# Performance work log

Hardware: AMD Instinct MI355X
Metric: run time of the kernel (lower is better)

The kernel has to match this reference:

```python
import math
import jax, jax.numpy as jnp
import numpy as np

B, H, W = 2, 128, 128
HW = H * W
D, NH, NL, KS = 256, 8, 1, 5
NP = KS * KS
HD = D // NH
DFF = 1024
KEEP = 0.25
H_SIZE = 188.0
EPS = 1e-5


def _layernorm(x, g, b):
    m = x.mean(-1, keepdims=True)
    v = ((x - m) ** 2).mean(-1, keepdims=True)
    return (x - m) * jax.lax.rsqrt(v + EPS) * g + b


def _mha(q_in, k_in, v_in, w_qkv, b_qkv, w_o, b_o):
    wq, wk, wv = jnp.split(w_qkv, 3, axis=0)
    bq, bk, bv = jnp.split(b_qkv, 3, axis=0)
    def heads(x, w, b):
        y = x @ w.T + b
        return y.reshape(y.shape[0], y.shape[1], NH, HD)
    q, k, v = heads(q_in, wq, bq), heads(k_in, wk, bk), heads(v_in, wv, bv)
    scores = jnp.einsum('bqhd,bkhd->bhqk', q, k) / math.sqrt(HD)
    attn = jax.nn.softmax(scores, axis=-1)
    out = jnp.einsum('bhqk,bkhd->bqhd', attn, v).reshape(q_in.shape[0], q_in.shape[1], D)
    return out @ w_o.T + b_o


def _bilinear(v, grid):
    # v: (B, HW, NH, HD); grid: (B, LQ, NH, NP, 2) normalized (x, y) in [0,1]
    x = grid[..., 0] * W - 0.5
    y = grid[..., 1] * H - 0.5
    x0 = jnp.floor(x); y0 = jnp.floor(y)
    lx = x - x0; ly = y - y0
    x0i = x0.astype(jnp.int32); y0i = y0.astype(jnp.int32)
    bidx = jnp.arange(v.shape[0])[:, None, None, None]
    hidx = jnp.arange(NH)[None, None, :, None]
    def corner(xi, yi, wgt):
        valid = (xi >= 0) & (xi < W) & (yi >= 0) & (yi < H)  # zero-pad outside
        idx = jnp.clip(yi, 0, H - 1) * W + jnp.clip(xi, 0, W - 1)
        s = v[bidx, idx, hidx]  # (B, LQ, NH, NP, HD)
        return s * (wgt * valid)[..., None]
    return (corner(x0i, y0i, (1 - lx) * (1 - ly))
            + corner(x0i + 1, y0i, lx * (1 - ly))
            + corner(x0i, y0i + 1, (1 - lx) * ly)
            + corner(x0i + 1, y0i + 1, lx * ly))


def _where_to_attend(query, ref_windows, lbw, lbb, sow, sob, kernel_indices):
    Bq, L = ref_windows.shape[:2]
    ob = (query @ lbw.T + lbb).reshape(Bq, L, NH, NL, 4)  # with_rotation=False -> 4 vars
    rw = ref_windows[:, :, None, None, :]  # (B, L, 1, 1, 7)
    ref_boxes = rw[..., jnp.array([0, 1, 3, 4])]
    ref_angles = rw[..., 6:7]
    angles = jnp.broadcast_to(ref_angles, (Bq, L, NH, NL, 1))
    boxes = ref_boxes + ob / 8.0 * ref_boxes[..., jnp.array([2, 3, 2, 3])]
    center = boxes[..., None, :2]  # (B, L, NH, NL, 1, 2)
    size = boxes[..., None, 2:]
    cos_a, sin_a = jnp.cos(angles), jnp.sin(angles)
    rot = jnp.stack([cos_a, -sin_a, sin_a, cos_a], -1).reshape(Bq, L, NH, NL, 1, 2, 2)
    dgrid = (query @ sow.T + sob).reshape(Bq, L, NH, NL, NP, 2) / H_SIZE
    fg = kernel_indices * jax.nn.relu(size)              # (B, L, NH, NL, NP, 2)
    fg = center + (fg[..., None, :] * rot).sum(-1)       # rotate then shift
    return fg + dgrid


def _box_attn(query, value, ref_windows, vpw, vpb, law, lab, lbw, lbb, sow, sob, ow, ob_, kernel_indices):
    Bq, LQ = query.shape[:2]
    LV = value.shape[1]
    v = (value @ vpw.T + vpb).reshape(Bq, LV, NH, HD)
    aw = jax.nn.softmax((query @ law.T + lab).reshape(Bq, LQ, NH, NL * NP), axis=-1)
    aw = aw.reshape(Bq, LQ, NH, NL, NP)
    grid = _where_to_attend(query, ref_windows, lbw, lbb, sow, sob, kernel_indices)
    sampled = _bilinear(v, grid[:, :, :, 0])             # single level (NL=1)
    out = (aw[:, :, :, 0, :, None] * sampled).sum(-2).reshape(Bq, LQ, D)
    return out @ ow.T + ob_


def _forward(src, pos, ref_windows, score_mask, in_proj_w, in_proj_b, mha_out_w, mha_out_b,
             value_proj_w, value_proj_b, linear_attn_w, linear_attn_b, linear_box_w, linear_box_b,
             samp_off_w, samp_off_b, ca_out_w, ca_out_b, lin1_w, lin1_b, lin2_w, lin2_b,
             qn_g, qn_b, n1_g, n1_b, n2_g, n2_b, kernel_indices):
    Bq = src.shape[0]
    fg_num = math.ceil(src.shape[1] * KEEP)
    sel_score, indices = jax.lax.top_k(score_mask, fg_num)
    gather = lambda x, i: jnp.take_along_axis(x, i[..., None], axis=1)
    sel_src = gather(src, indices)
    sel_pos = gather(pos, indices)
    sel_ref = gather(ref_windows, indices)
    q_num = math.ceil(fg_num * KEEP)
    q_idx = jax.lax.top_k(sel_score, q_num)[1]
    q_src = gather(sel_src, q_idx)
    q_pos = gather(sel_pos, q_idx)
    qk = q_src + q_pos
    q2 = _mha(qk, qk, q_src, in_proj_w, in_proj_b, mha_out_w, mha_out_b)
    q_src = _layernorm(q_src + q2, qn_g, qn_b)
    brow = jnp.arange(Bq)[:, None]
    sel_src = sel_src.at[brow, q_idx].set(q_src)
    src2 = _box_attn(sel_src + sel_pos, src, sel_ref, value_proj_w, value_proj_b,
                     linear_attn_w, linear_attn_b, linear_box_w, linear_box_b,
                     samp_off_w, samp_off_b, ca_out_w, ca_out_b, kernel_indices)
    sel_src = _layernorm(sel_src + src2, n1_g, n1_b)
    ff = jax.nn.relu(sel_src @ lin1_w.T + lin1_b) @ lin2_w.T + lin2_b
    sel_src = _layernorm(sel_src + ff, n2_g, n2_b)
    return src.at[brow, indices].set(sel_src)


def setup_inputs() -> dict:
    key = jax.random.key(0)
    ks = jax.random.split(key, 16)
    def w(k, shape):
        return jax.random.normal(k, shape, dtype=jnp.float32) * 0.02
    # deformable sampling-offsets bias init (per-head directional grid)
    thetas = np.arange(NH) * (2.0 * np.pi / NH)
    g = np.stack([np.cos(thetas), np.sin(thetas)], -1)
    g = g / np.abs(g).max(-1, keepdims=True)
    g = np.tile(g.reshape(NH, 1, 1, 2), (1, NL, NP, 1)) * (np.arange(NP) + 1).reshape(1, 1, NP, 1)
    samp_off_b = jnp.asarray(g.reshape(-1), dtype=jnp.float32)
    # fixed kernel indices buffer (odd kernel, (x,y) order, /kernel_size)
    ind = np.linspace(-(KS - 1) / 2, (KS - 1) / 2, KS)
    ii, jj = np.meshgrid(ind, ind, indexing='ij')
    kernel_indices = jnp.asarray(np.stack([jj, ii], -1).reshape(-1, 2) / KS, dtype=jnp.float32)
    return dict(
        src=jax.random.normal(ks[0], (B, HW, D), dtype=jnp.float32),
        pos=jax.random.normal(ks[1], (B, HW, D), dtype=jnp.float32),
        src_shape=jnp.array([[H, W]], dtype=jnp.int32),
        src_start_idx=jnp.zeros((1,), dtype=jnp.int32),
        ref_windows=jax.random.uniform(ks[2], (B, HW, 7), dtype=jnp.float32),
        score_mask=jax.random.normal(ks[3], (B, HW), dtype=jnp.float32),
        in_proj_w=w(ks[4], (3 * D, D)), in_proj_b=jnp.zeros((3 * D,), jnp.float32),
        mha_out_w=w(ks[5], (D, D)), mha_out_b=jnp.zeros((D,), jnp.float32),
        value_proj_w=w(ks[6], (D, D)), value_proj_b=jnp.zeros((D,), jnp.float32),
        linear_attn_w=w(ks[7], (NH * NL * NP, D)), linear_attn_b=jnp.zeros((NH * NL * NP,), jnp.float32),
        linear_box_w=w(ks[8], (NL * NH * 4, D)), linear_box_b=jnp.zeros((NL * NH * 4,), jnp.float32),
        samp_off_w=w(ks[9], (NH * NL * NP * 2, D)), samp_off_b=samp_off_b,
        ca_out_w=w(ks[10], (D, D)), ca_out_b=jnp.zeros((D,), jnp.float32),
        lin1_w=w(ks[11], (DFF, D)), lin1_b=jnp.zeros((DFF,), jnp.float32),
        lin2_w=w(ks[12], (D, DFF)), lin2_b=jnp.zeros((D,), jnp.float32),
        qn_g=jnp.ones((D,), jnp.float32), qn_b=jnp.zeros((D,), jnp.float32),
        n1_g=jnp.ones((D,), jnp.float32), n1_b=jnp.zeros((D,), jnp.float32),
        n2_g=jnp.ones((D,), jnp.float32), n2_b=jnp.zeros((D,), jnp.float32),
        kernel_indices=kernel_indices,
    )


def reference(src, pos, src_shape, src_start_idx, ref_windows, score_mask,
              in_proj_w, in_proj_b, mha_out_w, mha_out_b, value_proj_w, value_proj_b,
              linear_attn_w, linear_attn_b, linear_box_w, linear_box_b, samp_off_w, samp_off_b,
              ca_out_w, ca_out_b, lin1_w, lin1_b, lin2_w, lin2_b,
              qn_g, qn_b, n1_g, n1_b, n2_g, n2_b, kernel_indices):
    # src_shape/src_start_idx are static single-level metadata (H, W closed over)
    return _forward(src, pos, ref_windows, score_mask, in_proj_w, in_proj_b, mha_out_w, mha_out_b,
                    value_proj_w, value_proj_b, linear_attn_w, linear_attn_b, linear_box_w, linear_box_b,
                    samp_off_w, samp_off_b, ca_out_w, ca_out_b, lin1_w, lin1_b, lin2_w, lin2_b,
                    qn_g, qn_b, n1_g, n1_b, n2_g, n2_b, kernel_indices)
```

## Files before the change

kernel.cpp:

```cpp
#include <hip/hip_runtime.h>
#include <hip/hip_bf16.h>
#include <math.h>

#define HW_N   16384
#define DIM    256
#define NSEL   4096
#define NQ     1024
#define NHEAD  8
#define HD     32
#define NP_    25
#define DFF_   1024

#define OFF_SELREF  8448LL
#define OFF_SELSRC  65792LL
#define OFF_SELPOS  2162944LL
#define OFF_QUERY   4260096LL
#define OFF_BIG     6357248LL
#define OFF_WBF     10551552LL
#define OFF_F       14745856LL

__device__ __forceinline__ unsigned int f2s(float f) {
    unsigned int u = __float_as_uint(f);
    return (u & 0x80000000u) ? ~u : (u | 0x80000000u);
}

typedef __bf16 bf16x8 __attribute__((ext_vector_type(8)));
typedef __bf16 bf16x4 __attribute__((ext_vector_type(4)));
typedef float  f32x4  __attribute__((ext_vector_type(4)));

extern "C" __global__ __launch_bounds__(256)
void wcvt_kernel(const float* __restrict__ s0, const float* __restrict__ s1,
                 const float* __restrict__ s2, const float* __restrict__ s3,
                 const float* __restrict__ s4, const float* __restrict__ s5,
                 const float* __restrict__ s6, const float* __restrict__ s7,
                 const float* __restrict__ s8, __hip_bfloat16* __restrict__ dst) {
    const long long g = (long long)blockIdx.x * 256 + threadIdx.x;
    const float* s; long long base;
    if      (g < 196608)  { s = s0; base = 0; }
    else if (g < 262144)  { s = s1; base = 196608; }
    else if (g < 327680)  { s = s2; base = 262144; }
    else if (g < 378880)  { s = s3; base = 327680; }
    else if (g < 387072)  { s = s4; base = 378880; }
    else if (g < 489472)  { s = s5; base = 387072; }
    else if (g < 555008)  { s = s6; base = 489472; }
    else if (g < 817152)  { s = s7; base = 555008; }
    else                  { s = s8; base = 817152; }
    dst[g] = __float2bfloat16(s[g - base]);
}

extern "C" __global__ __launch_bounds__(512)
void topk_hist_kernel(const float* __restrict__ score, unsigned int* __restrict__ hist) {
    const int t = threadIdx.x, bx = blockIdx.x, bb = blockIdx.y;
    const int i = bx * 512 + t;
    unsigned int u = f2s(score[(long long)bb * HW_N + i]);
    atomicAdd(&hist[bb * 8192 + (u >> 19)], 1u);
}

extern "C" __global__ __launch_bounds__(1024)
void topk_scan_kernel(const unsigned int* __restrict__ hist, unsigned int* __restrict__ ctrl) {
    __shared__ unsigned int scan[1024];
    const int t = threadIdx.x, bb = blockIdx.x;
    unsigned int loc[8]; unsigned int lsum = 0u;
    #pragma unroll
    for (int k = 0; k < 8; ++k) { loc[k] = hist[bb * 8192 + t * 8 + k]; lsum += loc[k]; }
    scan[t] = lsum;
    __syncthreads();
    for (int off = 1; off < 1024; off <<= 1) {
        unsigned int v = (t + off < 1024) ? scan[t + off] : 0u;
        __syncthreads();
        scan[t] += v;
        __syncthreads();
    }
    unsigned int nxt = (t < 1023) ? scan[t + 1] : 0u;
    unsigned int run = nxt;
    for (int k = 7; k >= 0; --k) {
        run += loc[k];
        unsigned int above = run - loc[k];
        if (run >= 1024u && above < 1024u) { ctrl[bb * 16 + 0] = (unsigned)(t * 8 + k); ctrl[bb * 16 + 1] = 1024u - above; }
        if (run >= 4096u && above < 4096u) { ctrl[bb * 16 + 2] = (unsigned)(t * 8 + k); ctrl[bb * 16 + 3] = 4096u - above; }
    }
}

extern "C" __global__ __launch_bounds__(1024)
void topk_collect_kernel(const float* __restrict__ score, unsigned int* __restrict__ ctrl,
                         unsigned long long* __restrict__ list1,
                         unsigned long long* __restrict__ list2) {
    const int t = threadIdx.x, bx = blockIdx.x, bb = blockIdx.y;
    const int i = bx * 1024 + t;
    const unsigned int T1 = ctrl[bb * 16 + 0], T2 = ctrl[bb * 16 + 2];
    unsigned int u = f2s(score[(long long)bb * HW_N + i]);
    unsigned int bin = u >> 19;
    unsigned long long key = ((unsigned long long)u << 32) | (unsigned int)(~(unsigned int)i);
    if (bin == T1) {
        unsigned int p = atomicAdd(&ctrl[bb * 16 + 4], 1u);
        if (p < 2048u) list1[bb * 2048 + p] = key;
    }
    if (bin == T2 && T2 != T1) {
        unsigned int p = atomicAdd(&ctrl[bb * 16 + 5], 1u);
        if (p < 2048u) list2[bb * 2048 + p] = key;
    }
}

extern "C" __global__ __launch_bounds__(1024)
void topk_classify_kernel(const float* __restrict__ score, unsigned int* __restrict__ ctrl,
                          const unsigned long long* __restrict__ list1,
                          const unsigned long long* __restrict__ list2,
                          int* __restrict__ idx_out) {
    __shared__ unsigned int cA, cB, baseA, baseB;
    const int t = threadIdx.x, bx = blockIdx.x, bb = blockIdx.y;
    const int i = bx * 1024 + t;
    if (t == 0) { cA = 0u; cB = 0u; }
    __syncthreads();
    const unsigned int T1 = ctrl[bb * 16 + 0], need1 = ctrl[bb * 16 + 1];
    const unsigned int T2 = ctrl[bb * 16 + 2], need2 = ctrl[bb * 16 + 3];
    const unsigned int c1 = min(ctrl[bb * 16 + 4], 2048u);
    const unsigned int c2 = min(ctrl[bb * 16 + 5], 2048u);
    unsigned int u = f2s(score[(long long)bb * HW_N + i]);
    unsigned int bin = u >> 19;
    unsigned long long key = ((unsigned long long)u << 32) | (unsigned int)(~(unsigned int)i);
    bool inA = false, inB = false;
    if (bin > T1) {
        inA = true;
    } else if (bin == T1) {
        unsigned int r = 0;
        for (unsigned int q = 0; q < c1; ++q) r += (list1[bb * 2048 + q] > key) ? 1u : 0u;
        if (r < need1) inA = true;
        else if (T2 == T1) inB = (r < need2);
        else inB = true;
    } else if (bin > T2) {
        inB = true;
    } else if (bin == T2) {
        unsigned int r = 0;
        for (unsigned int q = 0; q < c2; ++q) r += (list2[bb * 2048 + q] > key) ? 1u : 0u;
        inB = (r < need2);
    }
    unsigned int sA = 0u, sB = 0u;
    if (inA) sA = atomicAdd(&cA, 1u);
    if (inB) sB = atomicAdd(&cB, 1u);
    __syncthreads();
    if (t == 0) {
        baseA = atomicAdd(&ctrl[bb * 16 + 6], cA);
        baseB = atomicAdd(&ctrl[bb * 16 + 7], cB);
    }
    __syncthreads();
    if (inA) idx_out[bb * NSEL + baseA + sA] = i;
    if (inB) idx_out[bb * NSEL + 1024 + baseB + sB] = i;
}

extern "C" __global__ __launch_bounds__(256)
void gather_kernel(const float* __restrict__ src, const float* __restrict__ pos,
                   const float* __restrict__ refw, const int* __restrict__ idx,
                   float* __restrict__ selsrc, float* __restrict__ selpos,
                   float* __restrict__ selref, float* __restrict__ qk) {
    const int s = blockIdx.x, bb = blockIdx.y, t = threadIdx.x;
    const int i = idx[bb * NSEL + s];
    const long long so = ((long long)(bb * NSEL + s)) * DIM;
    const long long go = ((long long)(bb * HW_N + i)) * DIM;
    float sv = src[go + t], pv = pos[go + t];
    selsrc[so + t] = sv;
    selpos[so + t] = pv;
    if (s < NQ) qk[((long long)(bb * NQ + s)) * DIM + t] = sv + pv;
    if (t < 7)
        selref[(long long)(bb * NSEL + s) * 7 + t] = refw[(long long)(bb * HW_N + i) * 7 + t];
}

extern "C" __global__ __launch_bounds__(256)
void gemm_kernel(const void* __restrict__ Avp, long long sA,
                 const __hip_bfloat16* __restrict__ W, const float* __restrict__ bias,
                 float* __restrict__ C, long long sC,
                 int M, int N, int K, int relu, int omode, int amode) {
    __shared__ __hip_bfloat16 As[64][72];
    __shared__ __hip_bfloat16 Ws[64][72];
    const int t = threadIdx.x;
    const int n0 = blockIdx.x * 64, m0 = blockIdx.y * 64;
    const long long zoff = (long long)blockIdx.z * sC;
    const int lane = t & 63, wv = t >> 6;
    const int mw = (wv >> 1) * 32, nw = (wv & 1) * 32;
    const int fr = lane & 15;
    const int fk = (lane >> 4) * 8;
    const int sr = t >> 2;
    const int sk = (t & 3) * 16;

    f32x4 acc[2][2];
    #pragma unroll
    for (int i = 0; i < 2; ++i)
        #pragma unroll
        for (int j = 0; j < 2; ++j) acc[i][j] = {0.f, 0.f, 0.f, 0.f};

    const bool wok = (n0 + sr) < N;
    for (int k0 = 0; k0 < K; k0 += 64) {
        uint4 wa = make_uint4(0u, 0u, 0u, 0u), wb = make_uint4(0u, 0u, 0u, 0u);
        if (wok) {
            const __hip_bfloat16* wp = W + (long long)(n0 + sr) * K + k0 + sk;
            wa = *(const uint4*)wp;
            wb = *(const uint4*)(wp + 8);
        }
        if (amode) {
            const __hip_bfloat16* ap = (const __hip_bfloat16*)Avp
                + (long long)blockIdx.z * sA + (long long)(m0 + sr) * K + k0 + sk;
            uint4 aa = *(const uint4*)ap;
            uint4 ab = *(const uint4*)(ap + 8);
            __syncthreads();
            *(uint4*)&As[sr][sk] = aa;
            *(uint4*)&As[sr][sk + 8] = ab;
            *(uint4*)&Ws[sr][sk] = wa;
            *(uint4*)&Ws[sr][sk + 8] = wb;
        } else {
            const float* ap = (const float*)Avp
                + (long long)blockIdx.z * sA + (long long)(m0 + sr) * K + k0 + sk;
            float av[16];
            #pragma unroll
            for (int q = 0; q < 4; ++q) {
                float4 v = *(const float4*)(ap + q * 4);
                av[q * 4 + 0] = v.x; av[q * 4 + 1] = v.y; av[q * 4 + 2] = v.z; av[q * 4 + 3] = v.w;
            }
            __syncthreads();
            #pragma unroll
            for (int q = 0; q < 16; ++q) As[sr][sk + q] = __float2bfloat16(av[q]);
            *(uint4*)&Ws[sr][sk] = wa;
            *(uint4*)&Ws[sr][sk + 8] = wb;
        }
        __syncthreads();
        #pragma unroll
        for (int kk = 0; kk < 64; kk += 32) {
            bf16x8 a0 = *(const bf16x8*)&As[mw + fr][kk + fk];
            bf16x8 a1 = *(const bf16x8*)&As[mw + 16 + fr][kk + fk];
            bf16x8 b0 = *(const bf16x8*)&Ws[nw + fr][kk + fk];
            bf16x8 b1 = *(const bf16x8*)&Ws[nw + 16 + fr][kk + fk];
            acc[0][0] = __builtin_amdgcn_mfma_f32_16x16x32_bf16(a0, b0, acc[0][0], 0, 0, 0);
            acc[0][1] = __builtin_amdgcn_mfma_f32_16x16x32_bf16(a0, b1, acc[0][1], 0, 0, 0);
            acc[1][0] = __builtin_amdgcn_mfma_f32_16x16x32_bf16(a1, b0, acc[1][0], 0, 0, 0);
            acc[1][1] = __builtin_amdgcn_mfma_f32_16x16x32_bf16(a1, b1, acc[1][1], 0, 0, 0);
        }
    }
    const int crow = (lane >> 4) * 4;
    #pragma unroll
    for (int mi = 0; mi < 2; ++mi) {
        #pragma unroll
        for (int ni = 0; ni < 2; ++ni) {
            const int col = n0 + nw + ni * 16 + fr;
            if (col < N) {
                const float bv = bias ? bias[col] : 0.f;
                #pragma unroll
                for (int r = 0; r < 4; ++r) {
                    const int row = m0 + mw + mi * 16 + crow + r;
                    float v = acc[mi][ni][r] + bv;
                    if (relu) v = fmaxf(v, 0.f);
                    if (omode == 0) {
                        C[zoff + (long long)row * N + col] = v;
                    } else if (omode == 1) {
                        ((__hip_bfloat16*)C)[zoff + (long long)row * N + col] = __float2bfloat16(v);
                    } else if (omode == 2) {
                        ((__hip_bfloat16*)C)[zoff + (long long)col * M + row] = __float2bfloat16(v);
                    } else {
                        ((__hip_bfloat16*)C)[zoff + ((long long)(col >> 5) * 16384 + row) * 32 + (col & 31)]
                            = __float2bfloat16(v);
                    }
                }
            }
        }
    }
}

extern "C" __global__ __launch_bounds__(256)
void attn_kernel(const __hip_bfloat16* __restrict__ qkb,
                 const __hip_bfloat16* __restrict__ vT,
                 float* __restrict__ attout) {
    __shared__ __hip_bfloat16 pb[16][1048];
    __shared__ float redm[4][16];
    __shared__ float reds[4][16];
    __shared__ float redo[4][16][33];
    const int t = threadIdx.x;
    const int qt = blockIdx.x, h = blockIdx.y, bb = blockIdx.z;
    const int q0 = qt * 16;
    const int lane = t & 63, wv = t >> 6;
    const int fr = lane & 15, g = lane >> 4;
    const int kbase = wv * 256;
    const float scale = 0.17677669529663687f;

    bf16x8 qfrag = *(const bf16x8*)(qkb + ((long long)(bb * NQ + q0 + fr)) * 512 + h * HD + g * 8);

    f32x4 sfr[16];
    #pragma unroll
    for (int kt = 0; kt < 16; ++kt) {
        const int key0 = kbase + kt * 16;
        bf16x8 kf = *(const bf16x8*)(qkb + ((long long)(bb * NQ + key0 + fr)) * 512 + 256 + h * HD + g * 8);
        f32x4 z = {0.f, 0.f, 0.f, 0.f};
        sfr[kt] = __builtin_amdgcn_mfma_f32_16x16x32_bf16(qfrag, kf, z, 0, 0, 0);
    }
    #pragma unroll
    for (int kt = 0; kt < 16; ++kt)
        #pragma unroll
        for (int r = 0; r < 4; ++r) sfr[kt][r] *= scale;

    #pragma unroll
    for (int r = 0; r < 4; ++r) {
        float mx = -1e30f;
        #pragma unroll
        for (int kt = 0; kt < 16; ++kt) mx = fmaxf(mx, sfr[kt][r]);
        #pragma unroll
        for (int mm = 1; mm <= 8; mm <<= 1) mx = fmaxf(mx, __shfl_xor(mx, mm, 64));
        float sm = 0.f;
        #pragma unroll
        for (int kt = 0; kt < 16; ++kt) sm += expf(sfr[kt][r] - mx);
        #pragma unroll
        for (int mm = 1; mm <= 8; mm <<= 1) sm += __shfl_xor(sm, mm, 64);
        if (fr == 0) { redm[wv][4 * g + r] = mx; reds[wv][4 * g + r] = sm; }
    }
    __syncthreads();

    float gm[4], gl[4];
    #pragma unroll
    for (int r = 0; r < 4; ++r) {
        const int q = 4 * g + r;
        float mm = fmaxf(fmaxf(redm[0][q], redm[1][q]), fmaxf(redm[2][q], redm[3][q]));
        float ll = 0.f;
        #pragma unroll
        for (int w2 = 0; w2 < 4; ++w2) ll += reds[w2][q] * expf(redm[w2][q] - mm);
        gm[r] = mm; gl[r] = 1.f / ll;
    }
    #pragma unroll
    for (int kt = 0; kt < 16; ++kt) {
        #pragma unroll
        for (int r = 0; r < 4; ++r) {
            float p = expf(sfr[kt][r] - gm[r]) * gl[r];
            pb[4 * g + r][kbase + kt * 16 + fr] = __float2bfloat16(p);
        }
    }

    f32x4 o0 = {0.f, 0.f, 0.f, 0.f}, o1 = {0.f, 0.f, 0.f, 0.f};
    const __hip_bfloat16* vbase = vT + ((long long)bb * DIM + h * HD) * 1024;
    #pragma unroll
    for (int ks = 0; ks < 8; ++ks) {
        const int key0 = kbase + ks * 32 + g * 8;
        bf16x8 pf = *(const bf16x8*)&pb[fr][key0];
        bf16x8 v0 = *(const bf16x8*)(vbase + (long long)fr * 1024 + key0);
        bf16x8 v1 = *(const bf16x8*)(vbase + (long long)(16 + fr) * 1024 + key0);
        o0 = __builtin_amdgcn_mfma_f32_16x16x32_bf16(pf, v0, o0, 0, 0, 0);
        o1 = __builtin_amdgcn_mfma_f32_16x16x32_bf16(pf, v1, o1, 0, 0, 0);
    }

    #pragma unroll
    for (int r = 0; r < 4; ++r) {
        redo[wv][4 * g + r][fr] = o0[r];
        redo[wv][4 * g + r][16 + fr] = o1[r];
    }
    __syncthreads();
    #pragma unroll
    for (int i = 0; i < 2; ++i) {
        const int idx = t + i * 256;
        const int q = idx >> 5, d = idx & 31;
        float v = redo[0][q][d] + redo[1][q][d] + redo[2][q][d] + redo[3][q][d];
        attout[((long long)(bb * NQ + q0 + q)) * DIM + h * HD + d] = v;
    }
}

extern "C" __global__ __launch_bounds__(256)
void ln_kernel(const float* __restrict__ X, long long sx,
               const float* __restrict__ R, long long sr,
               const float* __restrict__ g, const float* __restrict__ bta,
               float* __restrict__ O, long long so) {
    __shared__ float red[4];
    const int row = blockIdx.x, bb = blockIdx.y, t = threadIdx.x;
    float x = X[(long long)bb * sx + (long long)row * DIM + t]
            + R[(long long)bb * sr + (long long)row * DIM + t];
    float v = x;
    #pragma unroll
    for (int m = 32; m >= 1; m >>= 1) v += __shfl_xor(v, m, 64);
    if ((t & 63) == 0) red[t >> 6] = v;
    __syncthreads();
    float mean = (red[0] + red[1] + red[2] + red[3]) * (1.f / 256.f);
    __syncthreads();
    float d = x - mean;
    v = d * d;
    #pragma unroll
    for (int m = 32; m >= 1; m >>= 1) v += __shfl_xor(v, m, 64);
    if ((t & 63) == 0) red[t >> 6] = v;
    __syncthreads();
    float var = (red[0] + red[1] + red[2] + red[3]) * (1.f / 256.f);
    O[(long long)bb * so + (long long)row * DIM + t] = d * rsqrtf(var + 1e-5f) * g[t] + bta[t];
}

extern "C" __global__ __launch_bounds__(256)
void addq_kernel(const float* __restrict__ a, const float* __restrict__ b2, float* __restrict__ o) {
    long long i = (long long)blockIdx.x * 256 + threadIdx.x;
    o[i] = a[i] + b2[i];
}

extern "C" __global__ __launch_bounds__(256)
void boxattn_kernel(const float* __restrict__ aw, const float* __restrict__ ob,
                    const float* __restrict__ dgrid, const float* __restrict__ selref,
                    const __hip_bfloat16* __restrict__ vp, const float* __restrict__ kidx,
                    float* __restrict__ boxout) {
    __shared__ float aw_s[200];
    __shared__ float ob_s[32];
    __shared__ float ref_s[7];
    __shared__ float ki_s[50];
    __shared__ float box_s[8][6];
    __shared__ float mx_s[8];
    __shared__ float inv_s[8];
    __shared__ float wq_s[200];
    __shared__ int   i4_s[800];
    __shared__ float w4_s[800];
    __shared__ float red4[4][8][32];
    const int t = threadIdx.x;
    const int s = blockIdx.x, bb = blockIdx.y;
    const long long base = (long long)(bb * NSEL + s);
    if (t < 200) aw_s[t] = aw[base * 200 + t];
    if (t < 32)  ob_s[t] = ob[base * 32 + t];
    if (t < 7)   ref_s[t] = selref[base * 7 + t];
    if (t < 50)  ki_s[t] = kidx[t];
    __syncthreads();

    if (t < 8) {
        float mx = -1e30f;
        #pragma unroll
        for (int p = 0; p < NP_; ++p) mx = fmaxf(mx, aw_s[t * NP_ + p]);
        mx_s[t] = mx;
        const float r0 = ref_s[0], r1 = ref_s[1], r3 = ref_s[3], r4 = ref_s[4], r6 = ref_s[6];
        box_s[t][0] = r0 + ob_s[t * 4 + 0] * 0.125f * r3;
        box_s[t][1] = r1 + ob_s[t * 4 + 1] * 0.125f * r4;
        box_s[t][2] = fmaxf(r3 + ob_s[t * 4 + 2] * 0.125f * r3, 0.f);
        box_s[t][3] = fmaxf(r4 + ob_s[t * 4 + 3] * 0.125f * r4, 0.f);
        box_s[t][4] = cosf(r6);
        box_s[t][5] = sinf(r6);
    }
    __syncthreads();

    if (t < 200) {
        const int h = t / NP_, p = t - h * NP_;
        const float w = expf(aw_s[t] - mx_s[h]);
        wq_s[t] = w;
        const float cx = box_s[h][0], cy = box_s[h][1];
        const float sw = box_s[h][2], sh = box_s[h][3];
        const float ca = box_s[h][4], sa = box_s[h][5];
        const float fx = ki_s[p * 2 + 0] * sw;
        const float fy = ki_s[p * 2 + 1] * sh;
        const float gx = cx + ca * fx - sa * fy + dgrid[base * 400 + 2 * t + 0] * (1.f / 188.f);
        const float gy = cy + sa * fx + ca * fy + dgrid[base * 400 + 2 * t + 1] * (1.f / 188.f);
        const float x = gx * 128.f - 0.5f;
        const float y = gy * 128.f - 0.5f;
        const float x0f = floorf(x), y0f = floorf(y);
        const float lx = x - x0f, ly = y - y0f;
        const int x0 = (int)x0f, y0 = (int)y0f;
        #pragma unroll
        for (int c = 0; c < 4; ++c) {
            const int xi = x0 + (c & 1);
            const int yi = y0 + (c >> 1);
            const float wgt = ((c & 1) ? lx : 1.f - lx) * ((c >> 1) ? ly : 1.f - ly);
            const bool valid = (xi >= 0) & (xi < 128) & (yi >= 0) & (yi < 128);
            const int cxi = min(max(xi, 0), 127);
            const int cyi = min(max(yi, 0), 127);
            i4_s[t * 4 + c] = cyi * 128 + cxi;
            w4_s[t * 4 + c] = w * (valid ? wgt : 0.f);
        }
    }
    __syncthreads();
    if (t < 8) {
        float sm = 0.f;
        #pragma unroll
        for (int p = 0; p < NP_; ++p) sm += wq_s[t * NP_ + p];
        inv_s[t] = 1.f / sm;
    }
    __syncthreads();

    {
        const int lane = t & 63, wv = t >> 6;
        const int h2 = lane >> 3, q = lane & 7;
        const __hip_bfloat16* vb = vp + ((long long)(bb * 8 + h2) * 16384) * 32 + q * 4;
        int   pix[25];
        float wls[25];
        #pragma unroll
        for (int u = 0; u < 25; ++u) {
            const int e = h2 * 100 + wv + u * 4;
            pix[u] = i4_s[e];
            wls[u] = w4_s[e];
        }
        bf16x4 vv[25];
        #pragma unroll
        for (int u = 0; u < 25; ++u)
            vv[u] = *(const bf16x4*)(vb + (long long)pix[u] * 32);
        __builtin_amdgcn_sched_barrier(0);
        float a0 = 0.f, a1 = 0.f, a2 = 0.f, a3 = 0.f;
        #pragma unroll
        for (int u = 0; u < 25; ++u) {
            a0 += wls[u] * (float)vv[u][0];
            a1 += wls[u] * (float)vv[u][1];
            a2 += wls[u] * (float)vv[u][2];
            a3 += wls[u] * (float)vv[u][3];
        }
        red4[wv][h2][q * 4 + 0] = a0;
        red4[wv][h2][q * 4 + 1] = a1;
        red4[wv][h2][q * 4 + 2] = a2;
        red4[wv][h2][q * 4 + 3] = a3;
    }
    __syncthreads();
    {
        const int h = t >> 5, d = t & 31;
        float v = red4[0][h][d] + red4[1][h][d] + red4[2][h][d] + red4[3][h][d];
        boxout[base * DIM + h * HD + d] = v * inv_s[h];
    }
}

extern "C" __global__ __launch_bounds__(256)
void scatter_kernel(const int* __restrict__ idx, const float* __restrict__ sel,
                    float* __restrict__ out) {
    const int s = blockIdx.x, bb = blockIdx.y, t = threadIdx.x;
    const int i = idx[bb * NSEL + s];
    out[((long long)(bb * HW_N + i)) * DIM + t] = sel[((long long)(bb * NSEL + s)) * DIM + t];
}

extern "C" void kernel_launch(void* const* d_in, const int* in_sizes, int n_in,
                              void* d_out, int out_size, void* d_ws, size_t ws_size,
                              hipStream_t stream) {
    const float* src          = (const float*)d_in[0];
    const float* pos          = (const float*)d_in[1];
    const float* refw         = (const float*)d_in[4];
    const float* score        = (const float*)d_in[5];
    const float* in_proj_w    = (const float*)d_in[6];
    const float* in_proj_b    = (const float*)d_in[7];
    const float* mha_out_w    = (const float*)d_in[8];
    const float* mha_out_b    = (const float*)d_in[9];
    const float* value_proj_w = (const float*)d_in[10];
    const float* value_proj_b = (const float*)d_in[11];
    const float* lin_attn_w   = (const float*)d_in[12];
    const float* lin_attn_b   = (const float*)d_in[13];
    const float* lin_box_w    = (const float*)d_in[14];
    const float* lin_box_b    = (const float*)d_in[15];
    const float* samp_off_w   = (const float*)d_in[16];
    const float* samp_off_b   = (const float*)d_in[17];
    const float* ca_out_w     = (const float*)d_in[18];
    const float* ca_out_b     = (const float*)d_in[19];
    const float* lin1_w       = (const float*)d_in[20];
    const float* lin1_b       = (const float*)d_in[21];
    const float* lin2_w       = (const float*)d_in[22];
    const float* lin2_b       = (const float*)d_in[23];
    const float* qn_g         = (const float*)d_in[24];
    const float* qn_b         = (const float*)d_in[25];
    const float* n1_g         = (const float*)d_in[26];
    const float* n1_b         = (const float*)d_in[27];
    const float* n2_g         = (const float*)d_in[28];
    const float* n2_b         = (const float*)d_in[29];
    const float* kidx         = (const float*)d_in[30];

    float* w = (float*)d_ws;
    int* idxp = (int*)d_ws;
    float* selref = w + OFF_SELREF;
    float* selsrc = w + OFF_SELSRC;
    float* selpos = w + OFF_SELPOS;
    float* boxout = w + OFF_SELPOS;
    float* query  = w + OFF_QUERY;
    float* src2   = w + OFF_QUERY;
    __hip_bfloat16* vproj  = (__hip_bfloat16*)(w + OFF_BIG);
    __hip_bfloat16* ffntb  = (__hip_bfloat16*)(w + OFF_BIG);
    __hip_bfloat16* wbf    = (__hip_bfloat16*)(w + OFF_WBF);
    float* qk     = w + OFF_F;
    __hip_bfloat16* qkb = (__hip_bfloat16*)(w + OFF_F + 524288);
    __hip_bfloat16* vT  = (__hip_bfloat16*)(w + OFF_F + 1572864);
    float* attout = w + OFF_F + 2097152;
    float* q2     = w + OFF_F + 2621440;
    float* aw     = w + OFF_F;
    float* obuf   = w + OFF_F + 1638400;
    float* dgrid  = w + OFF_F + 1900544;
    float* ff     = w + OFF_F;
    unsigned int* hist2 = (unsigned int*)(w + OFF_F);
    unsigned int* ctrl2 = hist2 + 16384;
    unsigned long long* list1 = (unsigned long long*)(hist2 + 16448);
    unsigned long long* list2 = list1 + 2 * 2048;
    float* out    = (float*)d_out;

    const long long W_INPROJ = 0, W_MHAOUT = 196608, W_VALUE = 262144,
                    W_LATTN = 327680, W_LBOX = 378880, W_SOFF = 387072,
                    W_CAOUT = 489472, W_LIN1 = 555008, W_LIN2 = 817152;

    hipMemcpyAsync(d_out, src, (size_t)2 * HW_N * DIM * sizeof(float),
                   hipMemcpyDeviceToDevice, stream);

    wcvt_kernel<<<4216, 256, 0, stream>>>(in_proj_w, mha_out_w, value_proj_w,
                                          lin_attn_w, lin_box_w, samp_off_w,
                                          ca_out_w, lin1_w, lin2_w, wbf);

    hipMemsetAsync(hist2, 0, 16448 * sizeof(unsigned int), stream);
    topk_hist_kernel<<<dim3(32, 2), 512, 0, stream>>>(score, hist2);
    topk_scan_kernel<<<2, 1024, 0, stream>>>(hist2, ctrl2);
    topk_collect_kernel<<<dim3(16, 2), 1024, 0, stream>>>(score, ctrl2, list1, list2);
    topk_classify_kernel<<<dim3(16, 2), 1024, 0, stream>>>(score, ctrl2, list1, list2, idxp);

    gather_kernel<<<dim3(NSEL, 2), 256, 0, stream>>>(src, pos, refw, idxp,
                                                     selsrc, selpos, selref, qk);
    gemm_kernel<<<dim3(8, 16, 2), 256, 0, stream>>>(qk, 262144LL, wbf + W_INPROJ, in_proj_b,
                                                    (float*)qkb, 524288LL, NQ, 512, 256, 0, 1, 0);
    gemm_kernel<<<dim3(4, 16, 2), 256, 0, stream>>>(selsrc, 1048576LL, wbf + W_INPROJ + 512 * 256,
                                                    in_proj_b + 512, (float*)vT, 262144LL, NQ, 256, 256, 0, 2, 0);
    attn_kernel<<<dim3(64, 8, 2), 256, 0, stream>>>(qkb, vT, attout);
    gemm_kernel<<<dim3(4, 16, 2), 256, 0, stream>>>(attout, 262144LL, wbf + W_MHAOUT, mha_out_b,
                                                    q2, 262144LL, NQ, 256, 256, 0, 0, 0);
    ln_kernel<<<dim3(NQ, 2), 256, 0, stream>>>(selsrc, 1048576LL, q2, 262144LL,
                                               qn_g, qn_b, selsrc, 1048576LL);
    addq_kernel<<<8192, 256, 0, stream>>>(selsrc, selpos, query);
    gemm_kernel<<<dim3(4, 256, 2), 256, 0, stream>>>(src, 4194304LL, wbf + W_VALUE, value_proj_b,
                                                     (float*)vproj, 4194304LL, HW_N, 256, 256, 0, 3, 0);
    gemm_kernel<<<dim3(4, 64, 2), 256, 0, stream>>>(query, 1048576LL, wbf + W_LATTN, lin_attn_b,
                                                    aw, 819200LL, NSEL, 200, 256, 0, 0, 0);
    gemm_kernel<<<dim3(1, 64, 2), 256, 0, stream>>>(query, 1048576LL, wbf + W_LBOX, lin_box_b,
                                                    obuf, 131072LL, NSEL, 32, 256, 0, 0, 0);
    gemm_kernel<<<dim3(7, 64, 2), 256, 0, stream>>>(query, 1048576LL, wbf + W_SOFF, samp_off_b,
                                                    dgrid, 1638400LL, NSEL, 400, 256, 0, 0, 0);
    boxattn_kernel<<<dim3(NSEL, 2), 256, 0, stream>>>(aw, obuf, dgrid, selref, vproj, kidx, boxout);
    gemm_kernel<<<dim3(4, 64, 2), 256, 0, stream>>>(boxout, 1048576LL, wbf + W_CAOUT, ca_out_b,
                                                    src2, 1048576LL, NSEL, 256, 256, 0, 0, 0);
    ln_kernel<<<dim3(NSEL, 2), 256, 0, stream>>>(selsrc, 1048576LL, src2, 1048576LL,
                                                 n1_g, n1_b, selsrc, 1048576LL);
    gemm_kernel<<<dim3(16, 64, 2), 256, 0, stream>>>(selsrc, 1048576LL, wbf + W_LIN1, lin1_b,
                                                     (float*)ffntb, 4194304LL, NSEL, DFF_, 256, 1, 1, 0);
    gemm_kernel<<<dim3(4, 64, 2), 256, 0, stream>>>(ffntb, 4194304LL, wbf + W_LIN2, lin2_b,
                                                    ff, 1048576LL, NSEL, 256, DFF_, 0, 0, 1);
    ln_kernel<<<dim3(NSEL, 2), 256, 0, stream>>>(selsrc, 1048576LL, ff, 1048576LL,
                                                 n2_g, n2_b, selsrc, 1048576LL);
    scatter_kernel<<<dim3(NSEL, 2), 256, 0, stream>>>(idxp, selsrc, out);
}
```

Before: 457.1 us.

## Alias attention LDS buffers, batch loads before MFMA, reuse softmax exponentials

The attention kernel now shares one LDS buffer between the probability tile and the output-reduction scratch, with an added barrier to separate the two uses. This lowers shared memory per block, and launch bounds now request 4 blocks per CU. K and V/P fragment loads are grouped ahead of their MFMAs behind sched_barrier so memory latency can overlap. Softmax keeps the exponentials from the first pass and rescales them, using fast __expf, instead of recomputing exp. This adds register pressure from the batched fragments and slightly changes numerics.

```diff
diff --git a/kernel.cpp b/kernel.cpp
--- a/kernel.cpp
+++ b/kernel.cpp
@@ -262,14 +262,15 @@
     }
 }
 
-extern "C" __global__ __launch_bounds__(256)
+extern "C" __global__ __launch_bounds__(256, 4)
 void attn_kernel(const __hip_bfloat16* __restrict__ qkb,
                  const __hip_bfloat16* __restrict__ vT,
                  float* __restrict__ attout) {
-    __shared__ __hip_bfloat16 pb[16][1048];
+    __shared__ float sbuf[8256];
     __shared__ float redm[4][16];
     __shared__ float reds[4][16];
-    __shared__ float redo[4][16][33];
+    __hip_bfloat16 (*pb)[1032] = (__hip_bfloat16 (*)[1032])sbuf;
+    float (*redo)[16][33] = (float (*)[16][33])sbuf;
     const int t = threadIdx.x;
     const int qt = blockIdx.x, h = blockIdx.y, bb = blockIdx.z;
     const int q0 = qt * 16;
@@ -282,17 +283,26 @@
 
     f32x4 sfr[16];
     #pragma unroll
-    for (int kt = 0; kt < 16; ++kt) {
-        const int key0 = kbase + kt * 16;
-        bf16x8 kf = *(const bf16x8*)(qkb + ((long long)(bb * NQ + key0 + fr)) * 512 + 256 + h * HD + g * 8);
-        f32x4 z = {0.f, 0.f, 0.f, 0.f};
-        sfr[kt] = __builtin_amdgcn_mfma_f32_16x16x32_bf16(qfrag, kf, z, 0, 0, 0);
+    for (int half = 0; half < 2; ++half) {
+        bf16x8 kf[8];
+        #pragma unroll
+        for (int j = 0; j < 8; ++j) {
+            const int key0 = kbase + (half * 8 + j) * 16;
+            kf[j] = *(const bf16x8*)(qkb + ((long long)(bb * NQ + key0 + fr)) * 512 + 256 + h * HD + g * 8);
+        }
+        __builtin_amdgcn_sched_barrier(0);
+        #pragma unroll
+        for (int j = 0; j < 8; ++j) {
+            f32x4 z = {0.f, 0.f, 0.f, 0.f};
+            sfr[half * 8 + j] = __builtin_amdgcn_mfma_f32_16x16x32_bf16(qfrag, kf[j], z, 0, 0, 0);
+        }
     }
     #pragma unroll
     for (int kt = 0; kt < 16; ++kt)
         #pragma unroll
         for (int r = 0; r < 4; ++r) sfr[kt][r] *= scale;
 
+    float mxr[4];
     #pragma unroll
     for (int r = 0; r < 4; ++r) {
         float mx = -1e30f;
@@ -302,44 +312,57 @@
         for (int mm = 1; mm <= 8; mm <<= 1) mx = fmaxf(mx, __shfl_xor(mx, mm, 64));
         float sm = 0.f;
         #pragma unroll
-        for (int kt = 0; kt < 16; ++kt) sm += expf(sfr[kt][r] - mx);
+        for (int kt = 0; kt < 16; ++kt) {
+            float e = __expf(sfr[kt][r] - mx);
+            sfr[kt][r] = e;
+            sm += e;
+        }
         #pragma unroll
         for (int mm = 1; mm <= 8; mm <<= 1) sm += __shfl_xor(sm, mm, 64);
+        mxr[r] = mx;
         if (fr == 0) { redm[wv][4 * g + r] = mx; reds[wv][4 * g + r] = sm; }
     }
     __syncthreads();
 
-    float gm[4], gl[4];
+    float scl[4];
     #pragma unroll
     for (int r = 0; r < 4; ++r) {
         const int q = 4 * g + r;
         float mm = fmaxf(fmaxf(redm[0][q], redm[1][q]), fmaxf(redm[2][q], redm[3][q]));
         float ll = 0.f;
         #pragma unroll
-        for (int w2 = 0; w2 < 4; ++w2) ll += reds[w2][q] * expf(redm[w2][q] - mm);
-        gm[r] = mm; gl[r] = 1.f / ll;
+        for (int w2 = 0; w2 < 4; ++w2) ll += reds[w2][q] * __expf(redm[w2][q] - mm);
+        scl[r] = __expf(mxr[r] - mm) / ll;
     }
     #pragma unroll
     for (int kt = 0; kt < 16; ++kt) {
         #pragma unroll
         for (int r = 0; r < 4; ++r) {
-            float p = expf(sfr[kt][r] - gm[r]) * gl[r];
-            pb[4 * g + r][kbase + kt * 16 + fr] = __float2bfloat16(p);
+            pb[4 * g + r][kbase + kt * 16 + fr] = __float2bfloat16(sfr[kt][r] * scl[r]);
         }
     }
 
     f32x4 o0 = {0.f, 0.f, 0.f, 0.f}, o1 = {0.f, 0.f, 0.f, 0.f};
     const __hip_bfloat16* vbase = vT + ((long long)bb * DIM + h * HD) * 1024;
     #pragma unroll
-    for (int ks = 0; ks < 8; ++ks) {
-        const int key0 = kbase + ks * 32 + g * 8;
-        bf16x8 pf = *(const bf16x8*)&pb[fr][key0];
-        bf16x8 v0 = *(const bf16x8*)(vbase + (long long)fr * 1024 + key0);
-        bf16x8 v1 = *(const bf16x8*)(vbase + (long long)(16 + fr) * 1024 + key0);
-        o0 = __builtin_amdgcn_mfma_f32_16x16x32_bf16(pf, v0, o0, 0, 0, 0);
-        o1 = __builtin_amdgcn_mfma_f32_16x16x32_bf16(pf, v1, o1, 0, 0, 0);
-    }
-
+    for (int ksb = 0; ksb < 2; ++ksb) {
+        bf16x8 pf[4], v0[4], v1[4];
+        #pragma unroll
+        for (int j = 0; j < 4; ++j) {
+            const int key0 = kbase + (ksb * 4 + j) * 32 + g * 8;
+            pf[j] = *(const bf16x8*)&pb[fr][key0];
+            v0[j] = *(const bf16x8*)(vbase + (long long)fr * 1024 + key0);
+            v1[j] = *(const bf16x8*)(vbase + (long long)(16 + fr) * 1024 + key0);
+        }
+        __builtin_amdgcn_sched_barrier(0);
+        #pragma unroll
+        for (int j = 0; j < 4; ++j) {
+            o0 = __builtin_amdgcn_mfma_f32_16x16x32_bf16(pf[j], v0[j], o0, 0, 0, 0);
+            o1 = __builtin_amdgcn_mfma_f32_16x16x32_bf16(pf[j], v1[j], o1, 0, 0, 0);
+        }
+    }
+
+    __syncthreads();
     #pragma unroll
     for (int r = 0; r < 4; ++r) {
         redo[wv][4 * g + r][fr] = o0[r];
```

After: 442.3 us. 3.2% less time.
